# Performance work log

Measured on AMD Instinct MI355X. Metric: run time of the kernel, lower is better.

The kernel has to match this reference:

```python
import jax, jax.numpy as jnp
import numpy as np


def _soft_proto(x, P):
    d2 = (x * x).sum(-1, keepdims=True) - 2.0 * (x @ P.T) + (P * P).sum(-1)
    w = jax.nn.softmax(-d2, axis=-1)  # scores = -dist_sq, softmax over K
    return w @ P  # soft-matched prototypes


def setup_inputs() -> dict:
    key = jax.random.key(0)
    ks = jax.random.split(key, 12)
    B = 1024
    def u(k, shape, s=0.1):
        return jax.random.uniform(k, shape, minval=-s, maxval=s, dtype=jnp.float32)
    return {
        "fcn": jax.random.normal(ks[0], (B, 90, 90), jnp.float32),
        "scn": jax.random.normal(ks[1], (B, 90, 90), jnp.float32),
        # node embedding Linear(90->48), weights stored [in,out]
        "W_node": u(ks[2], (90, 48)), "b_node": jnp.zeros((48,), jnp.float32),
        "P_node": u(ks[3], (64, 48)),   # node prototypes, init uniform(-0.1,0.1)
        "W_graph": u(ks[4], (48, 32)), "b_graph": jnp.zeros((32,), jnp.float32),
        "P_graph": u(ks[5], (32, 32)),
        "Wg1": u(ks[6], (32, 32)), "bg1": jnp.zeros((32,), jnp.float32),
        "Wg2": u(ks[7], (32, 16)), "bg2": jnp.zeros((16,), jnp.float32),
        "P_cls": u(ks[8], (16, 16)),
        # classifier: final_dim = 2*90*48 + 2*32 + 2*16 = 8736
        "Wc1": u(ks[9], (8736, 256)), "bc1": jnp.zeros((256,), jnp.float32),
        "Wc2": u(ks[10], (256, 3)), "bc2": jnp.zeros((3,), jnp.float32),
    }


def reference(fcn, scn, W_node, b_node, P_node, W_graph, b_graph, P_graph,
              Wg1, bg1, Wg2, bg2, P_cls, Wc1, bc1, Wc2, bc2):
    def branch(x):
        nodes = x @ W_node + b_node                  # [B,90,48]
        nm = _soft_proto(nodes, P_node)              # [B,90,48]
        eg = nm.mean(axis=1) @ W_graph + b_graph     # [B,32]
        gp = _soft_proto(eg, P_graph)                # [B,32]
        ec = jax.nn.relu(gp @ Wg1 + bg1) @ Wg2 + bg2 # [B,16]
        cp = _soft_proto(ec, P_cls)                  # [B,16]
        return nm, gp, cp

    nmf, gpf, cpf = branch(fcn)
    nms, gps, cps = branch(scn)
    B = fcn.shape[0]
    R = jnp.concatenate(
        [nmf.reshape(B, -1), nms.reshape(B, -1), gpf, gps, cpf, cps], axis=-1)  # [B,8736]
    # dropout(0.5) is identity in eval mode
    logits = jax.nn.relu(R @ Wc1 + bc1) @ Wc2 + bc2  # [B,3]
    return logits
```

## Files before the change

### kernel.cpp

```cpp
#include <hip/hip_runtime.h>
#include <hip/hip_bf16.h>

using f16   = _Float16;
using f16x4 = __attribute__((ext_vector_type(4))) _Float16;
using f16x8 = __attribute__((ext_vector_type(8))) _Float16;
using f32x4 = __attribute__((ext_vector_type(4))) float;

__global__ __launch_bounds__(256) void prep_kernel(
    const float* __restrict__ Wn, const float* __restrict__ Pn,
    f16* __restrict__ wf, float* __restrict__ q)
{
  int i = blockIdx.x * 256 + threadIdx.x;
  if (i < 4992) {
    int n = i / 104, k = i - n * 104;
    wf[i] = (k < 90) ? (f16)Wn[k * 48 + n] : (f16)0.f;
  } else if (i < 8576) {
    int j = i - 4992; int p = j / 56, c = j - p * 56;
    wf[i] = (c < 48) ? (f16)Pn[p * 48 + c] : (f16)0.f;
  } else if (i < 12032) {
    int j = i - 8576; int r = j / 72, p = j - r * 72;
    wf[i] = (p < 64) ? (f16)Pn[p * 48 + r] : (f16)0.f;
  } else if (i < 12096) {
    int p = i - 12032;
    float s = 0.f;
    for (int j = 0; j < 48; ++j) { float v = Pn[p * 48 + j]; s = fmaf(v, v, s); }
    q[p] = s;
  }
}

__global__ __launch_bounds__(256) void wc1t_kernel(
    const float* __restrict__ Wc1, f16* __restrict__ Wc1T)
{
  __shared__ f16 sT[32 * 36];
  const int tid = threadIdx.x;
  const int kt = blockIdx.x, ct = blockIdx.y;
  const int c = tid & 31, r4 = (tid >> 5) * 4;
  #pragma unroll
  for (int i = 0; i < 4; ++i) {
    int r = r4 + i;
    sT[c * 36 + r] = (f16)Wc1[(size_t)(kt * 32 + r) * 256 + ct * 32 + c];
  }
  __syncthreads();
  #pragma unroll
  for (int i = 0; i < 4; ++i) {
    int r = r4 + i;
    Wc1T[(size_t)(ct * 32 + r) * 8736 + kt * 32 + c] = sT[r * 36 + c];
  }
}

__global__ __launch_bounds__(256, 6) void node_kernel(
    const float* __restrict__ fcn, const float* __restrict__ scn,
    const float* __restrict__ bn, const f16* __restrict__ wf,
    const float* __restrict__ qg,
    f16* __restrict__ R, float* __restrict__ nmmean)
{
  __shared__ __align__(16) f16 sW[96 * 72];
  __shared__ __align__(16) f16 sNodes[96 * 56];
  __shared__ float sQ[64];
  __shared__ float sMean[96];

  const f16* Pw   = wf + 4992;
  const f16* PnTw = wf + 8576;

  const int tid = threadIdx.x;
  const int lane = tid & 63, wv = tid >> 6;
  const int l15 = lane & 15, lg = lane >> 4;
  const int b = blockIdx.x, br = blockIdx.y;
  const float* x = (br ? scn : fcn) + (size_t)b * 8100;

  if (tid < 64) sQ[tid] = qg[tid];

  for (int mt = wv; mt < 6; mt += 4) {
    const int row = mt * 16 + l15;
    const float* xrow = x + row * 90;
    f16x8 a[3];
    #pragma unroll
    for (int kt = 0; kt < 3; ++kt) {
      const int k0 = kt * 32 + lg * 8;
      f16x8 h;
      #pragma unroll
      for (int e = 0; e < 8; ++e) h[e] = (f16)0.f;
      if (row < 90) {
        const float* src = xrow + k0;
        if (k0 < 88) {
          float2 u0 = *(const float2*)(src + 0);
          float2 u1 = *(const float2*)(src + 2);
          float2 u2 = *(const float2*)(src + 4);
          float2 u3 = *(const float2*)(src + 6);
          h[0] = (f16)u0.x; h[1] = (f16)u0.y; h[2] = (f16)u1.x; h[3] = (f16)u1.y;
          h[4] = (f16)u2.x; h[5] = (f16)u2.y; h[6] = (f16)u3.x; h[7] = (f16)u3.y;
        } else {
          float2 u0 = *(const float2*)src;
          h[0] = (f16)u0.x; h[1] = (f16)u0.y;
        }
      }
      a[kt] = h;
    }
    #pragma unroll
    for (int nt = 0; nt < 3; ++nt) {
      f32x4 acc = {0.f, 0.f, 0.f, 0.f};
      #pragma unroll
      for (int kt = 0; kt < 3; ++kt) {
        f16x8 bb = *(const f16x8*)&wf[(nt * 16 + l15) * 104 + kt * 32 + lg * 8];
        acc = __builtin_amdgcn_mfma_f32_16x16x32_f16(a[kt], bb, acc, 0, 0, 0);
      }
      const float bias = bn[nt * 16 + l15];
      #pragma unroll
      for (int r = 0; r < 4; ++r)
        sNodes[(mt * 16 + lg * 4 + r) * 56 + nt * 16 + l15] = (f16)(acc[r] + bias);
    }
  }
  __syncthreads();

  for (int mt = wv; mt < 6; mt += 4) {
    f32x4 acc[4];
    #pragma unroll
    for (int nt = 0; nt < 4; ++nt) acc[nt] = (f32x4){0.f, 0.f, 0.f, 0.f};
    const f16x8 a0 = *(const f16x8*)&sNodes[(mt * 16 + l15) * 56 + lg * 8];
    const f16x4 a1 = *(const f16x4*)&sNodes[(mt * 16 + l15) * 56 + 32 + lg * 4];
    #pragma unroll
    for (int nt = 0; nt < 4; ++nt) {
      f16x8 b0 = *(const f16x8*)&Pw[(nt * 16 + l15) * 56 + lg * 8];
      acc[nt] = __builtin_amdgcn_mfma_f32_16x16x32_f16(a0, b0, acc[nt], 0, 0, 0);
      f16x4 b1 = *(const f16x4*)&Pw[(nt * 16 + l15) * 56 + 32 + lg * 4];
      acc[nt] = __builtin_amdgcn_mfma_f32_16x16x16f16(a1, b1, acc[nt], 0, 0, 0);
    }
    float qv[4];
    #pragma unroll
    for (int nt = 0; nt < 4; ++nt) qv[nt] = sQ[nt * 16 + l15];
    #pragma unroll
    for (int r = 0; r < 4; ++r) {
      float s0 = 2.f * acc[0][r] - qv[0];
      float s1 = 2.f * acc[1][r] - qv[1];
      float s2 = 2.f * acc[2][r] - qv[2];
      float s3 = 2.f * acc[3][r] - qv[3];
      float m = fmaxf(fmaxf(s0, s1), fmaxf(s2, s3));
      m = fmaxf(m, __shfl_xor(m, 1, 64));
      m = fmaxf(m, __shfl_xor(m, 2, 64));
      m = fmaxf(m, __shfl_xor(m, 4, 64));
      m = fmaxf(m, __shfl_xor(m, 8, 64));
      float e0 = __expf(s0 - m), e1 = __expf(s1 - m);
      float e2 = __expf(s2 - m), e3 = __expf(s3 - m);
      float sum = (e0 + e1) + (e2 + e3);
      sum += __shfl_xor(sum, 1, 64);
      sum += __shfl_xor(sum, 2, 64);
      sum += __shfl_xor(sum, 4, 64);
      sum += __shfl_xor(sum, 8, 64);
      const float inv = 1.f / sum;
      const int row = mt * 16 + lg * 4 + r;
      sW[row * 72 + 0 * 16 + l15] = (f16)(e0 * inv);
      sW[row * 72 + 1 * 16 + l15] = (f16)(e1 * inv);
      sW[row * 72 + 2 * 16 + l15] = (f16)(e2 * inv);
      sW[row * 72 + 3 * 16 + l15] = (f16)(e3 * inv);
    }
  }
  __syncthreads();

  f16* Rrow = R + (size_t)b * 8736 + (size_t)br * 4320;
  for (int t = wv; t < 18; t += 4) {
    const int mt = t / 3, nt = t - 3 * mt;
    f32x4 acc = {0.f, 0.f, 0.f, 0.f};
    #pragma unroll
    for (int kt = 0; kt < 2; ++kt) {
      f16x8 a  = *(const f16x8*)&sW[(mt * 16 + l15) * 72 + kt * 32 + lg * 8];
      f16x8 bb = *(const f16x8*)&PnTw[(nt * 16 + l15) * 72 + kt * 32 + lg * 8];
      acc = __builtin_amdgcn_mfma_f32_16x16x32_f16(a, bb, acc, 0, 0, 0);
    }
    #pragma unroll
    for (int r = 0; r < 4; ++r) {
      const int row = mt * 16 + lg * 4 + r;
      const f16 hv = (f16)acc[r];
      sNodes[row * 56 + nt * 16 + l15] = hv;
      if (row < 90) Rrow[row * 48 + nt * 16 + l15] = hv;
    }
  }
  __syncthreads();

  if (tid < 96) {
    int j = tid < 48 ? tid : tid - 48;
    int h = tid < 48 ? 0 : 1;
    float s = 0.f;
    for (int i = h * 45; i < h * 45 + 45; ++i) s += (float)sNodes[i * 56 + j];
    sMean[tid] = s;
  }
  __syncthreads();
  if (tid < 48) {
    nmmean[((size_t)br * 1024 + b) * 48 + tid] =
        (sMean[tid] + sMean[48 + tid]) * (1.f / 90.f);
  }
}

__global__ __launch_bounds__(256) void graph_kernel(
    const float* __restrict__ nmmean,
    const float* __restrict__ Wg, const float* __restrict__ bg,
    const float* __restrict__ Pg,
    const float* __restrict__ Wg1, const float* __restrict__ bg1,
    const float* __restrict__ Wg2, const float* __restrict__ bg2,
    const float* __restrict__ Pc,
    f16* __restrict__ R)
{
  __shared__ float sE[4][64];
  __shared__ float sT[4][64];
  const int tid = threadIdx.x;
  const int wid = tid >> 6, lane = tid & 63;
  const int idx = blockIdx.x * 4 + wid;
  const int br = idx >> 10, b = idx & 1023;
  const float* mrow = nmmean + (size_t)idx * 48;
  f16* Rrow = R + (size_t)b * 8736;

  if (lane < 32) {
    float e = bg[lane];
    #pragma unroll
    for (int k = 0; k < 48; ++k) e = fmaf(mrow[k], Wg[k * 32 + lane], e);
    sE[wid][lane] = e;
  }
  __syncthreads();
  if (lane < 32) {
    float s = 0.f;
    #pragma unroll
    for (int j = 0; j < 32; ++j) { float pv = Pg[lane * 32 + j]; s += pv * (2.f * sE[wid][j] - pv); }
    float m = s;
    for (int d = 16; d >= 1; d >>= 1) m = fmaxf(m, __shfl_xor(m, d, 64));
    float ex = __expf(s - m);
    float sum = ex;
    for (int d = 16; d >= 1; d >>= 1) sum += __shfl_xor(sum, d, 64);
    sT[wid][lane] = ex / sum;
  }
  __syncthreads();
  if (lane < 32) {
    float g = 0.f;
    #pragma unroll
    for (int p = 0; p < 32; ++p) g = fmaf(sT[wid][p], Pg[p * 32 + lane], g);
    Rrow[8640 + br * 32 + lane] = (f16)g;
    sE[wid][lane] = g;
  }
  __syncthreads();
  if (lane < 32) {
    float h = bg1[lane];
    #pragma unroll
    for (int k = 0; k < 32; ++k) h = fmaf(sE[wid][k], Wg1[k * 32 + lane], h);
    sT[wid][lane] = fmaxf(h, 0.f);
  }
  __syncthreads();
  if (lane < 16) {
    float c = bg2[lane];
    #pragma unroll
    for (int k = 0; k < 32; ++k) c = fmaf(sT[wid][k], Wg2[k * 16 + lane], c);
    sE[wid][lane] = c;
  }
  __syncthreads();
  if (lane < 16) {
    float s = 0.f;
    #pragma unroll
    for (int j = 0; j < 16; ++j) { float pv = Pc[lane * 16 + j]; s += pv * (2.f * sE[wid][j] - pv); }
    float m = s;
    for (int d = 8; d >= 1; d >>= 1) m = fmaxf(m, __shfl_xor(m, d, 64));
    float ex = __expf(s - m);
    float sum = ex;
    for (int d = 8; d >= 1; d >>= 1) sum += __shfl_xor(sum, d, 64);
    sT[wid][lane] = ex / sum;
  }
  __syncthreads();
  if (lane < 16) {
    float c = 0.f;
    #pragma unroll
    for (int p = 0; p < 16; ++p) c = fmaf(sT[wid][p], Pc[p * 16 + lane], c);
    Rrow[8704 + br * 16 + lane] = (f16)c;
  }
}

__global__ __launch_bounds__(256) void gemm1_kernel(
    const f16* __restrict__ R, const f16* __restrict__ Wc1T,
    float* __restrict__ part, int KS)
{
  __shared__ __align__(16) f16 sA[128 * 40];
  __shared__ __align__(16) f16 sB[64 * 40];
  const int tid = threadIdx.x;
  const int lane = tid & 63, wv = tid >> 6;
  const int l15 = lane & 15, lg = lane >> 4;
  const int wm = wv >> 1, wn = wv & 1;
  const int bm = blockIdx.x * 128, bnc = blockIdx.y * 64, z = blockIdx.z;
  const int base = 273 / KS, rem = 273 - base * KS;
  const int t0 = z * base + (z < rem ? z : rem);
  const int nt_ = base + (z < rem ? 1 : 0);
  const int kbeg = t0 * 32, kend = (t0 + nt_) * 32;

  const int ar = tid >> 1, ah = (tid & 1) * 16;
  const int bc = tid >> 2, bh = (tid & 3) * 8;

  f32x4 acc[4][2];
  #pragma unroll
  for (int mt = 0; mt < 4; ++mt)
    #pragma unroll
    for (int nt = 0; nt < 2; ++nt) acc[mt][nt] = (f32x4){0.f, 0.f, 0.f, 0.f};

  for (int kk = kbeg; kk < kend; kk += 32) {
    const f16* asrc = &R[(size_t)(bm + ar) * 8736 + kk + ah];
    f16x8 v0 = *(const f16x8*)asrc;
    f16x8 v1 = *(const f16x8*)(asrc + 8);
    f16x8 w0 = *(const f16x8*)&Wc1T[(size_t)(bnc + bc) * 8736 + kk + bh];
    *(f16x8*)&sA[ar * 40 + ah] = v0;
    *(f16x8*)&sA[ar * 40 + ah + 8] = v1;
    *(f16x8*)&sB[bc * 40 + bh] = w0;
    __syncthreads();
    #pragma unroll
    for (int mt = 0; mt < 4; ++mt) {
      f16x8 a = *(const f16x8*)&sA[(wm * 64 + mt * 16 + l15) * 40 + lg * 8];
      #pragma unroll
      for (int nt = 0; nt < 2; ++nt) {
        f16x8 bb = *(const f16x8*)&sB[(wn * 32 + nt * 16 + l15) * 40 + lg * 8];
        acc[mt][nt] = __builtin_amdgcn_mfma_f32_16x16x32_f16(a, bb, acc[mt][nt], 0, 0, 0);
      }
    }
    __syncthreads();
  }
  float* pz = part + (size_t)z * 262144;
  #pragma unroll
  for (int mt = 0; mt < 4; ++mt)
    #pragma unroll
    for (int nt = 0; nt < 2; ++nt)
      #pragma unroll
      for (int r = 0; r < 4; ++r)
        pz[(size_t)(bm + wm * 64 + mt * 16 + lg * 4 + r) * 256 +
           bnc + wn * 32 + nt * 16 + l15] = acc[mt][nt][r];
}

__global__ __launch_bounds__(256) void head_kernel(
    const float* __restrict__ part, const float* __restrict__ bc1,
    const float* __restrict__ Wc2, const float* __restrict__ bc2,
    float* __restrict__ out, int KS)
{
  __shared__ float red[3][4];
  const int b = blockIdx.x, t = threadIdx.x;
  float acc = bc1[t];
  for (int z = 0; z < KS; ++z) acc += part[(size_t)z * 262144 + (size_t)b * 256 + t];
  float h = fmaxf(acc, 0.f);
  float p0 = h * Wc2[t * 3 + 0];
  float p1 = h * Wc2[t * 3 + 1];
  float p2 = h * Wc2[t * 3 + 2];
  for (int d = 32; d >= 1; d >>= 1) {
    p0 += __shfl_xor(p0, d, 64);
    p1 += __shfl_xor(p1, d, 64);
    p2 += __shfl_xor(p2, d, 64);
  }
  const int wid = t >> 6, lane = t & 63;
  if (lane == 0) { red[0][wid] = p0; red[1][wid] = p1; red[2][wid] = p2; }
  __syncthreads();
  if (t < 3) {
    out[(size_t)b * 3 + t] = red[t][0] + red[t][1] + red[t][2] + red[t][3] + bc2[t];
  }
}

extern "C" void kernel_launch(void* const* d_in, const int* in_sizes, int n_in,
                              void* d_out, int out_size, void* d_ws, size_t ws_size,
                              hipStream_t stream) {
  const float* fcn     = (const float*)d_in[0];
  const float* scn     = (const float*)d_in[1];
  const float* W_node  = (const float*)d_in[2];
  const float* b_node  = (const float*)d_in[3];
  const float* P_node  = (const float*)d_in[4];
  const float* W_graph = (const float*)d_in[5];
  const float* b_graph = (const float*)d_in[6];
  const float* P_graph = (const float*)d_in[7];
  const float* Wg1     = (const float*)d_in[8];
  const float* bg1     = (const float*)d_in[9];
  const float* Wg2     = (const float*)d_in[10];
  const float* bg2     = (const float*)d_in[11];
  const float* P_cls   = (const float*)d_in[12];
  const float* Wc1     = (const float*)d_in[13];
  const float* bc1     = (const float*)d_in[14];
  const float* Wc2     = (const float*)d_in[15];
  const float* bc2     = (const float*)d_in[16];
  float* out = (float*)d_out;

  char* ws = (char*)d_ws;
  f16*   R16    = (f16*)ws;
  f16*   Wc1T   = (f16*)(ws + 17891328);
  f16*   wf     = (f16*)(ws + 22364160);
  float* qbuf   = (float*)(ws + 22388224);
  float* nmmean = (float*)(ws + 22388480);
  float* part   = (float*)(ws + 22781696);

  size_t avail = ws_size > 22781696u ? ws_size - 22781696u : 0;
  int KS = (int)(avail / 1048576u);
  if (KS > 16) KS = 16;
  if (KS < 1) KS = 1;

  prep_kernel<<<48, 256, 0, stream>>>(W_node, P_node, wf, qbuf);
  wc1t_kernel<<<dim3(273, 8), 256, 0, stream>>>(Wc1, Wc1T);
  node_kernel<<<dim3(1024, 2), 256, 0, stream>>>(fcn, scn, b_node, wf, qbuf,
                                                 R16, nmmean);
  graph_kernel<<<512, 256, 0, stream>>>(nmmean, W_graph, b_graph, P_graph,
                                        Wg1, bg1, Wg2, bg2, P_cls, R16);
  gemm1_kernel<<<dim3(8, 4, KS), 256, 0, stream>>>(R16, Wc1T, part, KS);
  head_kernel<<<1024, 256, 0, stream>>>(part, bc1, Wc2, bc2, out, KS);
}
```

Baseline: 74.93 us.

## Fuse node column-sum into MFMA epilogue, prefetch GEMM tiles, unroll head reduction

The node kernel now builds the per-column node mean from register accumulators with cross-lane shuffles and a small shared buffer. This replaces the write to shared sNodes and the serial 45-row loop, along with one barrier. The classifier split-K GEMM loads the next K tile into registers before running the MFMAs on the current tile, so global load latency overlaps compute. The head kernel sums the split-K partials with four independent accumulators to expose more memory-level parallelism. Register pressure rises a little, and the floating-point summation order changes.

New measurement: 70.15 us. -6.4%, faster.

```diff
diff --git a/kernel.cpp b/kernel.cpp
--- a/kernel.cpp
+++ b/kernel.cpp
@@ -57,7 +57,7 @@
   __shared__ __align__(16) f16 sW[96 * 72];
   __shared__ __align__(16) f16 sNodes[96 * 56];
   __shared__ float sQ[64];
-  __shared__ float sMean[96];
+  __shared__ float sCol[4][3][16];
 
   const f16* Pw   = wf + 4992;
   const f16* PnTw = wf + 8576;
@@ -157,6 +157,7 @@
   __syncthreads();
 
   f16* Rrow = R + (size_t)b * 8736 + (size_t)br * 4320;
+  float cs[3] = {0.f, 0.f, 0.f};
   for (int t = wv; t < 18; t += 4) {
     const int mt = t / 3, nt = t - 3 * mt;
     f32x4 acc = {0.f, 0.f, 0.f, 0.f};
@@ -169,24 +170,27 @@
     #pragma unroll
     for (int r = 0; r < 4; ++r) {
       const int row = mt * 16 + lg * 4 + r;
-      const f16 hv = (f16)acc[r];
-      sNodes[row * 56 + nt * 16 + l15] = hv;
-      if (row < 90) Rrow[row * 48 + nt * 16 + l15] = hv;
-    }
-  }
-  __syncthreads();
-
-  if (tid < 96) {
-    int j = tid < 48 ? tid : tid - 48;
-    int h = tid < 48 ? 0 : 1;
-    float s = 0.f;
-    for (int i = h * 45; i < h * 45 + 45; ++i) s += (float)sNodes[i * 56 + j];
-    sMean[tid] = s;
+      if (row < 90) {
+        Rrow[row * 48 + nt * 16 + l15] = (f16)acc[r];
+        cs[nt] += acc[r];
+      }
+    }
+  }
+  #pragma unroll
+  for (int nt = 0; nt < 3; ++nt) {
+    cs[nt] += __shfl_xor(cs[nt], 16, 64);
+    cs[nt] += __shfl_xor(cs[nt], 32, 64);
+  }
+  if (lane < 16) {
+    sCol[wv][0][lane] = cs[0];
+    sCol[wv][1][lane] = cs[1];
+    sCol[wv][2][lane] = cs[2];
   }
   __syncthreads();
   if (tid < 48) {
-    nmmean[((size_t)br * 1024 + b) * 48 + tid] =
-        (sMean[tid] + sMean[48 + tid]) * (1.f / 90.f);
+    const int nt = tid >> 4, c = tid & 15;
+    float s = sCol[0][nt][c] + sCol[1][nt][c] + sCol[2][nt][c] + sCol[3][nt][c];
+    nmmean[((size_t)br * 1024 + b) * 48 + tid] = s * (1.f / 90.f);
   }
 }
 
@@ -294,15 +298,20 @@
     #pragma unroll
     for (int nt = 0; nt < 2; ++nt) acc[mt][nt] = (f32x4){0.f, 0.f, 0.f, 0.f};
 
+  f16x8 v0 = *(const f16x8*)&R[(size_t)(bm + ar) * 8736 + kbeg + ah];
+  f16x8 v1 = *(const f16x8*)&R[(size_t)(bm + ar) * 8736 + kbeg + ah + 8];
+  f16x8 w0 = *(const f16x8*)&Wc1T[(size_t)(bnc + bc) * 8736 + kbeg + bh];
+
   for (int kk = kbeg; kk < kend; kk += 32) {
-    const f16* asrc = &R[(size_t)(bm + ar) * 8736 + kk + ah];
-    f16x8 v0 = *(const f16x8*)asrc;
-    f16x8 v1 = *(const f16x8*)(asrc + 8);
-    f16x8 w0 = *(const f16x8*)&Wc1T[(size_t)(bnc + bc) * 8736 + kk + bh];
     *(f16x8*)&sA[ar * 40 + ah] = v0;
     *(f16x8*)&sA[ar * 40 + ah + 8] = v1;
     *(f16x8*)&sB[bc * 40 + bh] = w0;
     __syncthreads();
+    if (kk + 32 < kend) {
+      v0 = *(const f16x8*)&R[(size_t)(bm + ar) * 8736 + kk + 32 + ah];
+      v1 = *(const f16x8*)&R[(size_t)(bm + ar) * 8736 + kk + 32 + ah + 8];
+      w0 = *(const f16x8*)&Wc1T[(size_t)(bnc + bc) * 8736 + kk + 32 + bh];
+    }
     #pragma unroll
     for (int mt = 0; mt < 4; ++mt) {
       f16x8 a = *(const f16x8*)&sA[(wm * 64 + mt * 16 + l15) * 40 + lg * 8];
@@ -332,8 +341,16 @@
 {
   __shared__ float red[3][4];
   const int b = blockIdx.x, t = threadIdx.x;
-  float acc = bc1[t];
-  for (int z = 0; z < KS; ++z) acc += part[(size_t)z * 262144 + (size_t)b * 256 + t];
+  float s0 = 0.f, s1 = 0.f, s2 = 0.f, s3 = 0.f;
+  int z = 0;
+  for (; z + 4 <= KS; z += 4) {
+    s0 += part[(size_t)(z + 0) * 262144 + (size_t)b * 256 + t];
+    s1 += part[(size_t)(z + 1) * 262144 + (size_t)b * 256 + t];
+    s2 += part[(size_t)(z + 2) * 262144 + (size_t)b * 256 + t];
+    s3 += part[(size_t)(z + 3) * 262144 + (size_t)b * 256 + t];
+  }
+  for (; z < KS; ++z) s0 += part[(size_t)z * 262144 + (size_t)b * 256 + t];
+  float acc = bc1[t] + ((s0 + s1) + (s2 + s3));
   float h = fmaxf(acc, 0.f);
   float p0 = h * Wc2[t * 3 + 0];
   float p1 = h * Wc2[t * 3 + 1];
```
